# Optimization experiments

Measured on AMD Instinct MI355X. Metric: run time of the kernel, lower is better.

The kernel has to match this reference:

```python
import jax, jax.numpy as jnp
import numpy as np

N = 100000
FEAT = 256
HID = 128
OUT = 64
E = 1600000


def setup_inputs() -> dict:
    key = jax.random.key(0)
    ks = jax.random.split(key, 8)
    x = jax.random.normal(ks[0], (N, FEAT), dtype=jnp.float32)
    edge_index = jax.random.randint(ks[1], (2, E), 0, N, dtype=jnp.int64)
    # Glorot-like weights, zero bias (PyG GCNConv default init style)
    def glorot(k, fin, fout):
        s = (6.0 / (fin + fout)) ** 0.5
        return jax.random.uniform(k, (fin, fout), jnp.float32, -s, s)
    return {
        "x": x,
        "edge_index": edge_index,
        "W1": glorot(ks[2], FEAT, HID), "b1": jnp.zeros((HID,), jnp.float32),
        "W2": glorot(ks[3], HID, HID), "b2": jnp.zeros((HID,), jnp.float32),
        "W3": glorot(ks[4], HID, OUT), "b3": jnp.zeros((OUT,), jnp.float32),
    }


def _gcn_prep(edge_index, n_nodes):
    # Add self-loops and compute symmetric normalization deg^-1/2 (PyG gcn_norm).
    loops = jnp.arange(n_nodes, dtype=edge_index.dtype)
    src = jnp.concatenate([edge_index[0], loops])
    dst = jnp.concatenate([edge_index[1], loops])
    ones = jnp.ones(src.shape[0], dtype=jnp.float32)
    deg = jax.ops.segment_sum(ones, dst, num_segments=n_nodes)
    dinv = jnp.where(deg > 0, jax.lax.rsqrt(jnp.maximum(deg, 1.0)), 0.0)
    norm = dinv[src] * dinv[dst]  # [E+N]
    return src, dst, norm


def _gcn_layer(x, src, dst, norm, W, b, n_nodes):
    h = x @ W                              # [N, F_out]
    msg = h[src] * norm[:, None]           # gather + edge scale
    out = jax.ops.segment_sum(msg, dst, num_segments=n_nodes)  # scatter-add
    return out + b


def reference(x, edge_index, W1, b1, W2, b2, W3, b3):
    n = x.shape[0]
    src, dst, norm = _gcn_prep(edge_index, n)
    h = jax.nn.relu(_gcn_layer(x, src, dst, norm, W1, b1, n))
    h = jax.nn.relu(_gcn_layer(h, src, dst, norm, W2, b2, n))
    return _gcn_layer(h, src, dst, norm, W3, b3, n)
```

## Files before the change

kernel.cpp:

```cpp
#include <hip/hip_runtime.h>
#include <hip/hip_bf16.h>


#define NNODES 100000
#define NB 391
#define PB 2048
#define BCAP 12288

typedef _Float16 half8  __attribute__((ext_vector_type(8)));
typedef _Float16 half4v __attribute__((ext_vector_type(4)));
typedef float    floatx4 __attribute__((ext_vector_type(4)));

static __device__ __forceinline__ floatx4 h2f4(half4v v) {
    return (floatx4){(float)v.x, (float)v.y, (float)v.z, (float)v.w};
}
static __device__ __forceinline__ floatx4 h2f4lo(half8 v) {
    return (floatx4){(float)v[0], (float)v[1], (float)v[2], (float)v[3]};
}
static __device__ __forceinline__ floatx4 h2f4hi(half8 v) {
    return (floatx4){(float)v[4], (float)v[5], (float)v[6], (float)v[7]};
}

__global__ __launch_bounds__(256) void blockhist_k(const int* __restrict__ dst,
                                                   int* __restrict__ H, int e) {
    __shared__ int h[NB];
    for (int q = threadIdx.x; q < NB; q += 256) h[q] = 0;
    __syncthreads();
    int base = blockIdx.x * PB;
    int lim = e - base; if (lim > PB) lim = PB;
    for (int i = threadIdx.x; i < lim; i += 256)
        atomicAdd(&h[dst[base + i] >> 8], 1);
    __syncthreads();
    for (int q = threadIdx.x; q < NB; q += 256)
        H[(size_t)blockIdx.x * NB + q] = h[q];
}

__global__ __launch_bounds__(256) void bucketscan_k(const int* __restrict__ H,
                                                    int* __restrict__ O,
                                                    int* __restrict__ T, int npb) {
    __shared__ int lds[256];
    int b = blockIdx.x, t = threadIdx.x;
    int running = 0;
    for (int c0 = 0; c0 < npb; c0 += 256) {
        int idx = c0 + t;
        int v = (idx < npb) ? H[(size_t)idx * NB + b] : 0;
        lds[t] = v;
        __syncthreads();
        #pragma unroll
        for (int off = 1; off < 256; off <<= 1) {
            int u = (t >= off) ? lds[t - off] : 0;
            __syncthreads();
            lds[t] += u;
            __syncthreads();
        }
        int excl = lds[t] - v + running;
        if (idx < npb) O[(size_t)idx * NB + b] = excl;
        running += lds[255];
        __syncthreads();
    }
    if (t == 0) T[b] = running;
}

__global__ __launch_bounds__(512) void scanT_k(const int* __restrict__ T,
                                               int* __restrict__ bbase, int e) {
    __shared__ int lds[512];
    int t = threadIdx.x;
    int v = (t < NB) ? T[t] : 0;
    lds[t] = v;
    __syncthreads();
    #pragma unroll
    for (int off = 1; off < 512; off <<= 1) {
        int u = (t >= off) ? lds[t - off] : 0;
        __syncthreads();
        lds[t] += u;
        __syncthreads();
    }
    if (t < NB) bbase[t] = lds[t] - v;
    if (t == 0) bbase[NB] = e;
}

__global__ __launch_bounds__(256) void scatter_k(const int* __restrict__ src,
                                                 const int* __restrict__ dst,
                                                 const int* __restrict__ O,
                                                 const int* __restrict__ bbase,
                                                 unsigned* __restrict__ binned, int e) {
    __shared__ int cur[NB];
    for (int q = threadIdx.x; q < NB; q += 256)
        cur[q] = bbase[q] + O[(size_t)blockIdx.x * NB + q];
    __syncthreads();
    int base = blockIdx.x * PB;
    int lim = e - base; if (lim > PB) lim = PB;
    for (int i = threadIdx.x; i < lim; i += 256) {
        int d = dst[base + i];
        int s = src[base + i];
        int p = atomicAdd(&cur[d >> 8], 1);
        binned[p] = ((unsigned)(d & 255) << 17) | (unsigned)s;
    }
}

__global__ __launch_bounds__(256) void bucket_fill_k(
    const unsigned* __restrict__ binned, const int* __restrict__ bbase,
    int* __restrict__ rowptr, int* __restrict__ eidx,
    float* __restrict__ dinv, int n, int e) {
    __shared__ int cnt[256];
    __shared__ int cur[256];
    __shared__ int lds[256];
    __shared__ int sbuf[BCAP];
    int b = blockIdx.x, t = threadIdx.x;
    int beg = bbase[b], end = bbase[b + 1];
    int m = end - beg;
    cnt[t] = 0;
    __syncthreads();
    for (int q = t; q < m; q += 256) {
        unsigned r = binned[beg + q];
        atomicAdd(&cnt[r >> 17], 1);
    }
    __syncthreads();
    int v = cnt[t];
    lds[t] = v;
    __syncthreads();
    #pragma unroll
    for (int off = 1; off < 256; off <<= 1) {
        int u = (t >= off) ? lds[t - off] : 0;
        __syncthreads();
        lds[t] += u;
        __syncthreads();
    }
    int excl = lds[t] - v;
    int node = b * 256 + t;
    if (node < n) {
        rowptr[node] = beg + excl;
        dinv[node] = rsqrtf(1.0f + (float)v);
    }
    if (b == NB - 1 && t == 0) rowptr[n] = e;
    cur[t] = excl;
    __syncthreads();
    for (int q = t; q < m; q += 256) {
        unsigned r = binned[beg + q];
        int p = atomicAdd(&cur[r >> 17], 1);
        if (p < BCAP) sbuf[p] = (int)(r & 0x1FFFFu);
    }
    __syncthreads();
    for (int q = t; q < m; q += 256) eidx[beg + q] = sbuf[q];
}

static __device__ __forceinline__ void cast_frag(
    const float* __restrict__ W, _Float16* __restrict__ Wf,
    int FIN, int FOUT, int i) {
    int k = i / FOUT, n = i % FOUT;
    int ct = n >> 4, mrow = n & 15;
    int kc = k >> 5, hi = (k & 31) >> 3, j = k & 7;
    int NKC = FIN / 32;
    int idx = ((ct * NKC + kc) * 64 + hi * 16 + mrow) * 8 + j;
    Wf[idx] = (_Float16)W[(size_t)k * FOUT + n];
}

__global__ __launch_bounds__(256) void castW_k(
    const float* __restrict__ W1, const float* __restrict__ W2,
    const float* __restrict__ W3, _Float16* __restrict__ Wf1,
    _Float16* __restrict__ Wf2, _Float16* __restrict__ Wf3) {
    int i = blockIdx.x * 256 + threadIdx.x;
    if (i < 256 * 128) cast_frag(W1, Wf1, 256, 128, i);
    if (i < 128 * 128) cast_frag(W2, Wf2, 128, 128, i);
    if (i < 128 * 64)  cast_frag(W3, Wf3, 128, 64, i);
}

template<typename TA, int FIN, int FOUT>
__global__ __launch_bounds__(256, 2) void gemm_ldsB_k(
    const TA* __restrict__ X, const _Float16* __restrict__ Wf,
    const float* __restrict__ dinv, _Float16* __restrict__ G, int n)
{
    constexpr int NKC = FIN / 32;
    constexpr int NCT = FOUT / 16;
    __shared__ _Float16 wS[FOUT * FIN];

    const int tid  = threadIdx.x;
    const int wave = tid >> 6;
    const int lane = tid & 63;
    const int mrow = lane & 15;
    const int kq   = (lane >> 4) * 8;

    {
        const half8* s = (const half8*)Wf;
        half8* d = (half8*)wS;
        constexpr int TOT8 = FOUT * FIN / 8;
        #pragma unroll
        for (int i = tid; i < TOT8; i += 256) d[i] = s[i];
    }

    int r = blockIdx.x * 64 + wave * 16 + mrow;
    if (r > n - 1) r = n - 1;

    half8 af[NKC];
    if constexpr (sizeof(TA) == 4) {
        const float* xp = (const float*)X + (size_t)r * FIN + kq;
        float4 t0[NKC], t1[NKC];
        #pragma unroll
        for (int kc = 0; kc < NKC; ++kc) {
            t0[kc] = *(const float4*)(xp + kc * 32);
            t1[kc] = *(const float4*)(xp + kc * 32 + 4);
        }
        #pragma unroll
        for (int kc = 0; kc < NKC; ++kc) {
            float4 u0 = t0[kc], u1 = t1[kc];
            af[kc] = (half8){(_Float16)u0.x, (_Float16)u0.y, (_Float16)u0.z, (_Float16)u0.w,
                             (_Float16)u1.x, (_Float16)u1.y, (_Float16)u1.z, (_Float16)u1.w};
        }
    } else {
        const _Float16* xp = (const _Float16*)X + (size_t)r * FIN + kq;
        #pragma unroll
        for (int kc = 0; kc < NKC; ++kc)
            af[kc] = *(const half8*)(xp + kc * 32);
    }

    __syncthreads();

    floatx4 acc[NCT];
    #pragma unroll
    for (int ct = 0; ct < NCT; ++ct) acc[ct] = (floatx4){0.f, 0.f, 0.f, 0.f};

    #pragma unroll
    for (int kc = 0; kc < NKC; ++kc) {
        #pragma unroll
        for (int ct = 0; ct < NCT; ++ct) {
            half8 bf = *(const half8*)&wS[(((ct * NKC) + kc) * 64 + lane) * 8];
            acc[ct] = __builtin_amdgcn_mfma_f32_16x16x32_f16(af[kc], bf, acc[ct], 0, 0, 0);
        }
    }

    int rbase = blockIdx.x * 64 + wave * 16 + (lane >> 4) * 4;
    #pragma unroll
    for (int reg = 0; reg < 4; ++reg) {
        int rr = rbase + reg;
        if (rr < n) {
            float s = dinv[rr];
            #pragma unroll
            for (int ct = 0; ct < NCT; ++ct)
                G[(size_t)rr * FOUT + ct * 16 + mrow] = (_Float16)(acc[ct][reg] * s);
        }
    }
}

template<bool RELU>
__global__ __launch_bounds__(256) void gatherq128_k(
    const _Float16* __restrict__ g, const int* __restrict__ rowptr,
    const int* __restrict__ eidx, const float* __restrict__ dinv,
    const float* __restrict__ bias, _Float16* __restrict__ out, int n)
{
    const int wave = threadIdx.x >> 6;
    const int lane = threadIdx.x & 63;
    const int q = lane >> 4;
    const int f = lane & 15;
    const int node = blockIdx.x * 4 + wave;
    if (node >= n) return;

    const int beg = rowptr[node];
    const int end = rowptr[node + 1];

    const half8* g8 = (const half8*)g;
    floatx4 aA0 = {0.f,0.f,0.f,0.f}, aA1 = aA0, aB0 = aA0, aB1 = aA0;
    {
        half8 v = g8[(size_t)node * 16 + f];
        if (q == 0) { aA0 = h2f4lo(v); aA1 = h2f4hi(v); }
    }

    for (int j0 = beg; j0 < end; j0 += 64) {
        int m = end - j0; if (m > 64) m = 64;
        int id = (lane < m) ? __builtin_nontemporal_load(eidx + j0 + lane) : 0;
        int t = 0;
        for (; t + 15 < m; t += 16) {
            int i0 = __shfl(id, t + q);
            int i1 = __shfl(id, t + 4 + q);
            int i2 = __shfl(id, t + 8 + q);
            int i3 = __shfl(id, t + 12 + q);
            half8 v0 = g8[(size_t)i0 * 16 + f];
            half8 v1 = g8[(size_t)i1 * 16 + f];
            half8 v2 = g8[(size_t)i2 * 16 + f];
            half8 v3 = g8[(size_t)i3 * 16 + f];
            aA0 += h2f4lo(v0); aA1 += h2f4hi(v0);
            aB0 += h2f4lo(v1); aB1 += h2f4hi(v1);
            aA0 += h2f4lo(v2); aA1 += h2f4hi(v2);
            aB0 += h2f4lo(v3); aB1 += h2f4hi(v3);
        }
        for (; t < m; t += 4) {
            int e = t + q;
            int i0 = __shfl(id, e & 63);
            half8 v0 = g8[(size_t)i0 * 16 + f];
            if (e < m) { aA0 += h2f4lo(v0); aA1 += h2f4hi(v0); }
        }
    }

    aA0 += aB0; aA1 += aB1;
    #pragma unroll
    for (int off = 16; off <= 32; off <<= 1) {
        aA0.x += __shfl_xor(aA0.x, off);
        aA0.y += __shfl_xor(aA0.y, off);
        aA0.z += __shfl_xor(aA0.z, off);
        aA0.w += __shfl_xor(aA0.w, off);
        aA1.x += __shfl_xor(aA1.x, off);
        aA1.y += __shfl_xor(aA1.y, off);
        aA1.z += __shfl_xor(aA1.z, off);
        aA1.w += __shfl_xor(aA1.w, off);
    }

    if (q == 0) {
        float sc = dinv[node];
        float4 b0 = *(const float4*)(bias + 8 * f);
        float4 b1 = *(const float4*)(bias + 8 * f + 4);
        float o0 = fmaf(aA0.x, sc, b0.x);
        float o1 = fmaf(aA0.y, sc, b0.y);
        float o2 = fmaf(aA0.z, sc, b0.z);
        float o3 = fmaf(aA0.w, sc, b0.w);
        float o4 = fmaf(aA1.x, sc, b1.x);
        float o5 = fmaf(aA1.y, sc, b1.y);
        float o6 = fmaf(aA1.z, sc, b1.z);
        float o7 = fmaf(aA1.w, sc, b1.w);
        if (RELU) {
            o0 = fmaxf(o0, 0.f); o1 = fmaxf(o1, 0.f);
            o2 = fmaxf(o2, 0.f); o3 = fmaxf(o3, 0.f);
            o4 = fmaxf(o4, 0.f); o5 = fmaxf(o5, 0.f);
            o6 = fmaxf(o6, 0.f); o7 = fmaxf(o7, 0.f);
        }
        half8 hv = {(_Float16)o0, (_Float16)o1, (_Float16)o2, (_Float16)o3,
                    (_Float16)o4, (_Float16)o5, (_Float16)o6, (_Float16)o7};
        __builtin_nontemporal_store(hv, (half8*)out + (size_t)node * 16 + f);
    }
}

__global__ __launch_bounds__(256) void gatherq64_k(
    const _Float16* __restrict__ g, const int* __restrict__ rowptr,
    const int* __restrict__ eidx, const float* __restrict__ dinv,
    const float* __restrict__ bias, float* __restrict__ out, int n)
{
    const int wave = threadIdx.x >> 6;
    const int lane = threadIdx.x & 63;
    const int q = lane >> 4;
    const int f = lane & 15;
    const int node = blockIdx.x * 4 + wave;
    if (node >= n) return;

    const int beg = rowptr[node];
    const int end = rowptr[node + 1];

    const half4v* g4 = (const half4v*)g;
    floatx4 aA = {0.f,0.f,0.f,0.f}, aB = aA;
    {
        half4v v = g4[(size_t)node * 16 + f];
        if (q == 0) aA = h2f4(v);
    }

    for (int j0 = beg; j0 < end; j0 += 64) {
        int m = end - j0; if (m > 64) m = 64;
        int id = (lane < m) ? __builtin_nontemporal_load(eidx + j0 + lane) : 0;
        int t = 0;
        for (; t + 15 < m; t += 16) {
            int i0 = __shfl(id, t + q);
            int i1 = __shfl(id, t + 4 + q);
            int i2 = __shfl(id, t + 8 + q);
            int i3 = __shfl(id, t + 12 + q);
            half4v v0 = g4[(size_t)i0 * 16 + f];
            half4v v1 = g4[(size_t)i1 * 16 + f];
            half4v v2 = g4[(size_t)i2 * 16 + f];
            half4v v3 = g4[(size_t)i3 * 16 + f];
            aA += h2f4(v0); aB += h2f4(v1);
            aA += h2f4(v2); aB += h2f4(v3);
        }
        for (; t < m; t += 4) {
            int e = t + q;
            int i0 = __shfl(id, e & 63);
            half4v v0 = g4[(size_t)i0 * 16 + f];
            if (e < m) aA += h2f4(v0);
        }
    }

    aA += aB;
    #pragma unroll
    for (int off = 16; off <= 32; off <<= 1) {
        aA.x += __shfl_xor(aA.x, off);
        aA.y += __shfl_xor(aA.y, off);
        aA.z += __shfl_xor(aA.z, off);
        aA.w += __shfl_xor(aA.w, off);
    }

    if (q == 0) {
        float sc = dinv[node];
        float4 bb = *(const float4*)(bias + 4 * f);
        floatx4 o;
        o.x = fmaf(aA.x, sc, bb.x);
        o.y = fmaf(aA.y, sc, bb.y);
        o.z = fmaf(aA.z, sc, bb.z);
        o.w = fmaf(aA.w, sc, bb.w);
        __builtin_nontemporal_store(o, (floatx4*)(out + (size_t)node * 64 + 4 * f));
    }
}

extern "C" void kernel_launch(void* const* d_in, const int* in_sizes, int n_in,
                              void* d_out, int out_size, void* d_ws, size_t ws_size,
                              hipStream_t stream) {
    const float* x  = (const float*)d_in[0];
    const int*   ei = (const int*)d_in[1];
    const float* W1 = (const float*)d_in[2];
    const float* b1 = (const float*)d_in[3];
    const float* W2 = (const float*)d_in[4];
    const float* b2 = (const float*)d_in[5];
    const float* W3 = (const float*)d_in[6];
    const float* b3 = (const float*)d_in[7];
    float* out = (float*)d_out;

    const int N = NNODES;
    const int E = in_sizes[1] / 2;
    const int* srcI = ei;
    const int* dstI = ei + E;

    const int npb = (E + PB - 1) / PB;

    char* ws = (char*)d_ws;
    size_t p = 0;
    auto alloc = [&](size_t bytes) { void* r = ws + p; p = (p + bytes + 255) & ~(size_t)255; return r; };
    float*     dinv   = (float*)    alloc((size_t)N * 4);
    int*       rowptr = (int*)      alloc((size_t)(N + 1) * 4);
    int*       bbase  = (int*)      alloc((size_t)(NB + 1) * 4);
    int*       T      = (int*)      alloc((size_t)NB * 4);
    int*       H      = (int*)      alloc((size_t)npb * NB * 4);
    int*       O      = (int*)      alloc((size_t)npb * NB * 4);
    unsigned*  binned = (unsigned*) alloc((size_t)E * 4);
    int*       eidx   = (int*)      alloc((size_t)E * 4);
    _Float16*  Wf1    = (_Float16*) alloc((size_t)128 * 256 * 2);
    _Float16*  Wf2    = (_Float16*) alloc((size_t)128 * 128 * 2);
    _Float16*  Wf3    = (_Float16*) alloc((size_t)64 * 128 * 2);
    _Float16*  A      = (_Float16*) alloc((size_t)N * 128 * 2);
    _Float16*  Ch     = (_Float16*) alloc((size_t)N * 128 * 2);

    const int nb_node4 = (N + 3) / 4;
    const int nb_gemm  = (N + 63) / 64;

    blockhist_k<<<npb, 256, 0, stream>>>(dstI, H, E);
    castW_k<<<128, 256, 0, stream>>>(W1, W2, W3, Wf1, Wf2, Wf3);
    bucketscan_k<<<NB, 256, 0, stream>>>(H, O, T, npb);
    scanT_k<<<1, 512, 0, stream>>>(T, bbase, E);
    scatter_k<<<npb, 256, 0, stream>>>(srcI, dstI, O, bbase, binned, E);
    bucket_fill_k<<<NB, 256, 0, stream>>>(binned, bbase, rowptr, eidx, dinv, N, E);

    gemm_ldsB_k<float, 256, 128><<<nb_gemm, 256, 0, stream>>>(x, Wf1, dinv, A, N);
    gatherq128_k<true><<<nb_node4, 256, 0, stream>>>(A, rowptr, eidx, dinv, b1, Ch, N);

    gemm_ldsB_k<_Float16, 128, 128><<<nb_gemm, 256, 0, stream>>>(Ch, Wf2, dinv, A, N);
    gatherq128_k<true><<<nb_node4, 256, 0, stream>>>(A, rowptr, eidx, dinv, b2, Ch, N);

    gemm_ldsB_k<_Float16, 128, 64><<<nb_gemm, 256, 0, stream>>>(Ch, Wf3, dinv, A, N);
    gatherq64_k<<<nb_node4, 256, 0, stream>>>(A, rowptr, eidx, dinv, b3, out, N);
}
```

Measured before the change: 452.3 us.

## Make GEMM kernels persistent with prefetch of next row tile

Turns the three per-layer GEMM kernels into persistent kernels with a fixed grid (512 or 1024 blocks) that loop over 64-row tiles. The W fragment is loaded into LDS once per block instead of once per tile. The next tile's A rows are loaded into registers while the current tile's MFMAs run, hiding global load latency. The cost is higher register pressure from the prefetch buffers, and the launch-bounds occupancy hint now varies per layer.

```diff
diff --git a/kernel.cpp b/kernel.cpp
--- a/kernel.cpp
+++ b/kernel.cpp
@@ -165,8 +165,8 @@
     if (i < 128 * 64)  cast_frag(W3, Wf3, 128, 64, i);
 }
 
-template<typename TA, int FIN, int FOUT>
-__global__ __launch_bounds__(256, 2) void gemm_ldsB_k(
+template<typename TA, int FIN, int FOUT, int WPE>
+__global__ __launch_bounds__(256, WPE) void gemm_persist_k(
     const TA* __restrict__ X, const _Float16* __restrict__ Wf,
     const float* __restrict__ dinv, _Float16* __restrict__ G, int n)
 {
@@ -180,6 +180,27 @@
     const int mrow = lane & 15;
     const int kq   = (lane >> 4) * 8;
 
+    float4 t0[NKC], t1[NKC];
+    half8  araw[NKC];
+
+    auto issueA = [&](int tile) {
+        int r = tile * 64 + wave * 16 + mrow;
+        if (r > n - 1) r = n - 1;
+        if constexpr (sizeof(TA) == 4) {
+            const float* xp = (const float*)X + (size_t)r * FIN + kq;
+            #pragma unroll
+            for (int kc = 0; kc < NKC; ++kc) {
+                t0[kc] = *(const float4*)(xp + kc * 32);
+                t1[kc] = *(const float4*)(xp + kc * 32 + 4);
+            }
+        } else {
+            const _Float16* xp = (const _Float16*)X + (size_t)r * FIN + kq;
+            #pragma unroll
+            for (int kc = 0; kc < NKC; ++kc)
+                araw[kc] = *(const half8*)(xp + kc * 32);
+        }
+    };
+
     {
         const half8* s = (const half8*)Wf;
         half8* d = (half8*)wS;
@@ -187,56 +208,50 @@
         #pragma unroll
         for (int i = tid; i < TOT8; i += 256) d[i] = s[i];
     }
-
-    int r = blockIdx.x * 64 + wave * 16 + mrow;
-    if (r > n - 1) r = n - 1;
-
-    half8 af[NKC];
-    if constexpr (sizeof(TA) == 4) {
-        const float* xp = (const float*)X + (size_t)r * FIN + kq;
-        float4 t0[NKC], t1[NKC];
+    issueA(blockIdx.x);
+    __syncthreads();
+
+    const int ntiles = (n + 63) >> 6;
+    for (int tile = blockIdx.x; tile < ntiles; tile += gridDim.x) {
+        half8 af[NKC];
+        if constexpr (sizeof(TA) == 4) {
+            #pragma unroll
+            for (int kc = 0; kc < NKC; ++kc) {
+                float4 u0 = t0[kc], u1 = t1[kc];
+                af[kc] = (half8){(_Float16)u0.x, (_Float16)u0.y, (_Float16)u0.z, (_Float16)u0.w,
+                                 (_Float16)u1.x, (_Float16)u1.y, (_Float16)u1.z, (_Float16)u1.w};
+            }
+        } else {
+            #pragma unroll
+            for (int kc = 0; kc < NKC; ++kc) af[kc] = araw[kc];
+        }
+
+        int tn = tile + gridDim.x;
+        if (tn < ntiles) issueA(tn);
+
+        floatx4 acc[NCT];
+        #pragma unroll
+        for (int ct = 0; ct < NCT; ++ct) acc[ct] = (floatx4){0.f, 0.f, 0.f, 0.f};
+
         #pragma unroll
         for (int kc = 0; kc < NKC; ++kc) {
-            t0[kc] = *(const float4*)(xp + kc * 32);
-            t1[kc] = *(const float4*)(xp + kc * 32 + 4);
-        }
+            #pragma unroll
+            for (int ct = 0; ct < NCT; ++ct) {
+                half8 bf = *(const half8*)&wS[(((ct * NKC) + kc) * 64 + lane) * 8];
+                acc[ct] = __builtin_amdgcn_mfma_f32_16x16x32_f16(af[kc], bf, acc[ct], 0, 0, 0);
+            }
+        }
+
+        int rbase = tile * 64 + wave * 16 + (lane >> 4) * 4;
         #pragma unroll
-        for (int kc = 0; kc < NKC; ++kc) {
-            float4 u0 = t0[kc], u1 = t1[kc];
-            af[kc] = (half8){(_Float16)u0.x, (_Float16)u0.y, (_Float16)u0.z, (_Float16)u0.w,
-                             (_Float16)u1.x, (_Float16)u1.y, (_Float16)u1.z, (_Float16)u1.w};
-        }
-    } else {
-        const _Float16* xp = (const _Float16*)X + (size_t)r * FIN + kq;
-        #pragma unroll
-        for (int kc = 0; kc < NKC; ++kc)
-            af[kc] = *(const half8*)(xp + kc * 32);
-    }
-
-    __syncthreads();
-
-    floatx4 acc[NCT];
-    #pragma unroll
-    for (int ct = 0; ct < NCT; ++ct) acc[ct] = (floatx4){0.f, 0.f, 0.f, 0.f};
-
-    #pragma unroll
-    for (int kc = 0; kc < NKC; ++kc) {
-        #pragma unroll
-        for (int ct = 0; ct < NCT; ++ct) {
-            half8 bf = *(const half8*)&wS[(((ct * NKC) + kc) * 64 + lane) * 8];
-            acc[ct] = __builtin_amdgcn_mfma_f32_16x16x32_f16(af[kc], bf, acc[ct], 0, 0, 0);
-        }
-    }
-
-    int rbase = blockIdx.x * 64 + wave * 16 + (lane >> 4) * 4;
-    #pragma unroll
-    for (int reg = 0; reg < 4; ++reg) {
-        int rr = rbase + reg;
-        if (rr < n) {
-            float s = dinv[rr];
-            #pragma unroll
-            for (int ct = 0; ct < NCT; ++ct)
-                G[(size_t)rr * FOUT + ct * 16 + mrow] = (_Float16)(acc[ct][reg] * s);
+        for (int reg = 0; reg < 4; ++reg) {
+            int rr = rbase + reg;
+            if (rr < n) {
+                float s = dinv[rr];
+                #pragma unroll
+                for (int ct = 0; ct < NCT; ++ct)
+                    G[(size_t)rr * FOUT + ct * 16 + mrow] = (_Float16)(acc[ct][reg] * s);
+            }
         }
     }
 }
@@ -432,7 +447,8 @@
     _Float16*  Ch     = (_Float16*) alloc((size_t)N * 128 * 2);
 
     const int nb_node4 = (N + 3) / 4;
-    const int nb_gemm  = (N + 63) / 64;
+    const int GP2 = 512;
+    const int GP4 = 1024;
 
     blockhist_k<<<npb, 256, 0, stream>>>(dstI, H, E);
     castW_k<<<128, 256, 0, stream>>>(W1, W2, W3, Wf1, Wf2, Wf3);
@@ -441,12 +457,12 @@
     scatter_k<<<npb, 256, 0, stream>>>(srcI, dstI, O, bbase, binned, E);
     bucket_fill_k<<<NB, 256, 0, stream>>>(binned, bbase, rowptr, eidx, dinv, N, E);
 
-    gemm_ldsB_k<float, 256, 128><<<nb_gemm, 256, 0, stream>>>(x, Wf1, dinv, A, N);
+    gemm_persist_k<float, 256, 128, 2><<<GP2, 256, 0, stream>>>(x, Wf1, dinv, A, N);
     gatherq128_k<true><<<nb_node4, 256, 0, stream>>>(A, rowptr, eidx, dinv, b1, Ch, N);
 
-    gemm_ldsB_k<_Float16, 128, 128><<<nb_gemm, 256, 0, stream>>>(Ch, Wf2, dinv, A, N);
+    gemm_persist_k<_Float16, 128, 128, 4><<<GP4, 256, 0, stream>>>(Ch, Wf2, dinv, A, N);
     gatherq128_k<true><<<nb_node4, 256, 0, stream>>>(A, rowptr, eidx, dinv, b2, Ch, N);
 
-    gemm_ldsB_k<_Float16, 128, 64><<<nb_gemm, 256, 0, stream>>>(Ch, Wf3, dinv, A, N);
+    gemm_persist_k<_Float16, 128, 64, 4><<<GP4, 256, 0, stream>>>(Ch, Wf3, dinv, A, N);
     gatherq64_k<<<nb_node4, 256, 0, stream>>>(A, rowptr, eidx, dinv, b3, out, N);
 }
```

After: 523.4 us. 15.7% more time.

## Replace two-level bucket sort CSR build with global atomic histogram and scatter

Applied to the files above, without the earlier changes.

Replaces the bucketed radix-style CSR construction (per-block histograms, bucket scan, binned scatter, per-bucket LDS fill) with a per-node global atomic degree histogram, a two-level scan, and a direct atomic-cursor scatter of source indices into CSR order. This drops the intermediate binned array and the H/O tables, and zeroes the degree buffer inside the weight-cast kernel. In exchange it uses 1.6M global atomics twice, and edge order within each row becomes nondeterministic, which can cause small floating-point differences in the aggregation and worse locality in the gather.

```diff
diff --git a/kernel.cpp b/kernel.cpp
--- a/kernel.cpp
+++ b/kernel.cpp
@@ -4,8 +4,6 @@
 
 #define NNODES 100000
 #define NB 391
-#define PB 2048
-#define BCAP 12288
 
 typedef _Float16 half8  __attribute__((ext_vector_type(8)));
 typedef _Float16 half4v __attribute__((ext_vector_type(4)));
@@ -19,129 +17,6 @@
 }
 static __device__ __forceinline__ floatx4 h2f4hi(half8 v) {
     return (floatx4){(float)v[4], (float)v[5], (float)v[6], (float)v[7]};
-}
-
-__global__ __launch_bounds__(256) void blockhist_k(const int* __restrict__ dst,
-                                                   int* __restrict__ H, int e) {
-    __shared__ int h[NB];
-    for (int q = threadIdx.x; q < NB; q += 256) h[q] = 0;
-    __syncthreads();
-    int base = blockIdx.x * PB;
-    int lim = e - base; if (lim > PB) lim = PB;
-    for (int i = threadIdx.x; i < lim; i += 256)
-        atomicAdd(&h[dst[base + i] >> 8], 1);
-    __syncthreads();
-    for (int q = threadIdx.x; q < NB; q += 256)
-        H[(size_t)blockIdx.x * NB + q] = h[q];
-}
-
-__global__ __launch_bounds__(256) void bucketscan_k(const int* __restrict__ H,
-                                                    int* __restrict__ O,
-                                                    int* __restrict__ T, int npb) {
-    __shared__ int lds[256];
-    int b = blockIdx.x, t = threadIdx.x;
-    int running = 0;
-    for (int c0 = 0; c0 < npb; c0 += 256) {
-        int idx = c0 + t;
-        int v = (idx < npb) ? H[(size_t)idx * NB + b] : 0;
-        lds[t] = v;
-        __syncthreads();
-        #pragma unroll
-        for (int off = 1; off < 256; off <<= 1) {
-            int u = (t >= off) ? lds[t - off] : 0;
-            __syncthreads();
-            lds[t] += u;
-            __syncthreads();
-        }
-        int excl = lds[t] - v + running;
-        if (idx < npb) O[(size_t)idx * NB + b] = excl;
-        running += lds[255];
-        __syncthreads();
-    }
-    if (t == 0) T[b] = running;
-}
-
-__global__ __launch_bounds__(512) void scanT_k(const int* __restrict__ T,
-                                               int* __restrict__ bbase, int e) {
-    __shared__ int lds[512];
-    int t = threadIdx.x;
-    int v = (t < NB) ? T[t] : 0;
-    lds[t] = v;
-    __syncthreads();
-    #pragma unroll
-    for (int off = 1; off < 512; off <<= 1) {
-        int u = (t >= off) ? lds[t - off] : 0;
-        __syncthreads();
-        lds[t] += u;
-        __syncthreads();
-    }
-    if (t < NB) bbase[t] = lds[t] - v;
-    if (t == 0) bbase[NB] = e;
-}
-
-__global__ __launch_bounds__(256) void scatter_k(const int* __restrict__ src,
-                                                 const int* __restrict__ dst,
-                                                 const int* __restrict__ O,
-                                                 const int* __restrict__ bbase,
-                                                 unsigned* __restrict__ binned, int e) {
-    __shared__ int cur[NB];
-    for (int q = threadIdx.x; q < NB; q += 256)
-        cur[q] = bbase[q] + O[(size_t)blockIdx.x * NB + q];
-    __syncthreads();
-    int base = blockIdx.x * PB;
-    int lim = e - base; if (lim > PB) lim = PB;
-    for (int i = threadIdx.x; i < lim; i += 256) {
-        int d = dst[base + i];
-        int s = src[base + i];
-        int p = atomicAdd(&cur[d >> 8], 1);
-        binned[p] = ((unsigned)(d & 255) << 17) | (unsigned)s;
-    }
-}
-
-__global__ __launch_bounds__(256) void bucket_fill_k(
-    const unsigned* __restrict__ binned, const int* __restrict__ bbase,
-    int* __restrict__ rowptr, int* __restrict__ eidx,
-    float* __restrict__ dinv, int n, int e) {
-    __shared__ int cnt[256];
-    __shared__ int cur[256];
-    __shared__ int lds[256];
-    __shared__ int sbuf[BCAP];
-    int b = blockIdx.x, t = threadIdx.x;
-    int beg = bbase[b], end = bbase[b + 1];
-    int m = end - beg;
-    cnt[t] = 0;
-    __syncthreads();
-    for (int q = t; q < m; q += 256) {
-        unsigned r = binned[beg + q];
-        atomicAdd(&cnt[r >> 17], 1);
-    }
-    __syncthreads();
-    int v = cnt[t];
-    lds[t] = v;
-    __syncthreads();
-    #pragma unroll
-    for (int off = 1; off < 256; off <<= 1) {
-        int u = (t >= off) ? lds[t - off] : 0;
-        __syncthreads();
-        lds[t] += u;
-        __syncthreads();
-    }
-    int excl = lds[t] - v;
-    int node = b * 256 + t;
-    if (node < n) {
-        rowptr[node] = beg + excl;
-        dinv[node] = rsqrtf(1.0f + (float)v);
-    }
-    if (b == NB - 1 && t == 0) rowptr[n] = e;
-    cur[t] = excl;
-    __syncthreads();
-    for (int q = t; q < m; q += 256) {
-        unsigned r = binned[beg + q];
-        int p = atomicAdd(&cur[r >> 17], 1);
-        if (p < BCAP) sbuf[p] = (int)(r & 0x1FFFFu);
-    }
-    __syncthreads();
-    for (int q = t; q < m; q += 256) eidx[beg + q] = sbuf[q];
 }
 
 static __device__ __forceinline__ void cast_frag(
@@ -155,14 +30,91 @@
     Wf[idx] = (_Float16)W[(size_t)k * FOUT + n];
 }
 
-__global__ __launch_bounds__(256) void castW_k(
+__global__ __launch_bounds__(256) void castWz_k(
     const float* __restrict__ W1, const float* __restrict__ W2,
     const float* __restrict__ W3, _Float16* __restrict__ Wf1,
-    _Float16* __restrict__ Wf2, _Float16* __restrict__ Wf3) {
+    _Float16* __restrict__ Wf2, _Float16* __restrict__ Wf3,
+    int* __restrict__ deg) {
     int i = blockIdx.x * 256 + threadIdx.x;
+    for (int q = i; q < NNODES; q += 128 * 256) deg[q] = 0;
     if (i < 256 * 128) cast_frag(W1, Wf1, 256, 128, i);
     if (i < 128 * 128) cast_frag(W2, Wf2, 128, 128, i);
     if (i < 128 * 64)  cast_frag(W3, Wf3, 128, 64, i);
+}
+
+__global__ __launch_bounds__(256) void hist_k(const int* __restrict__ dst,
+                                              int* __restrict__ deg, int e) {
+    int i0 = blockIdx.x * 256 + threadIdx.x;
+    int stride = gridDim.x * 256;
+    for (int i = i0; i < e; i += stride)
+        atomicAdd(&deg[__builtin_nontemporal_load(dst + i)], 1);
+}
+
+__global__ __launch_bounds__(256) void blockscan_k(const int* __restrict__ deg,
+                                                   int* __restrict__ rowloc,
+                                                   int* __restrict__ T, int n) {
+    __shared__ int lds[256];
+    int b = blockIdx.x, t = threadIdx.x;
+    int node = b * 256 + t;
+    int v = (node < n) ? deg[node] : 0;
+    lds[t] = v;
+    __syncthreads();
+    #pragma unroll
+    for (int off = 1; off < 256; off <<= 1) {
+        int u = (t >= off) ? lds[t - off] : 0;
+        __syncthreads();
+        lds[t] += u;
+        __syncthreads();
+    }
+    if (node < n) rowloc[node] = lds[t] - v;
+    if (t == 255) T[b] = lds[255];
+}
+
+__global__ __launch_bounds__(512) void scanT_k(const int* __restrict__ T,
+                                               int* __restrict__ bbase, int e) {
+    __shared__ int lds[512];
+    int t = threadIdx.x;
+    int v = (t < NB) ? T[t] : 0;
+    lds[t] = v;
+    __syncthreads();
+    #pragma unroll
+    for (int off = 1; off < 512; off <<= 1) {
+        int u = (t >= off) ? lds[t - off] : 0;
+        __syncthreads();
+        lds[t] += u;
+        __syncthreads();
+    }
+    if (t < NB) bbase[t] = lds[t] - v;
+    if (t == 0) bbase[NB] = e;
+}
+
+__global__ __launch_bounds__(256) void finalize_k(
+    const int* __restrict__ deg, const int* __restrict__ rowloc,
+    const int* __restrict__ bbase, int* __restrict__ rowptr,
+    int* __restrict__ cursor, float* __restrict__ dinv, int n, int e) {
+    int b = blockIdx.x, t = threadIdx.x;
+    int node = b * 256 + t;
+    if (node < n) {
+        int rp = bbase[b] + rowloc[node];
+        rowptr[node] = rp;
+        cursor[node] = rp;
+        dinv[node] = rsqrtf(1.0f + (float)deg[node]);
+    }
+    if (b == NB - 1 && t == 0) rowptr[n] = e;
+}
+
+__global__ __launch_bounds__(256) void scatterg_k(const int* __restrict__ src,
+                                                  const int* __restrict__ dst,
+                                                  int* __restrict__ cursor,
+                                                  int* __restrict__ eidx, int e) {
+    int i0 = blockIdx.x * 256 + threadIdx.x;
+    int stride = gridDim.x * 256;
+    for (int i = i0; i < e; i += stride) {
+        int d = __builtin_nontemporal_load(dst + i);
+        int s = __builtin_nontemporal_load(src + i);
+        int p = atomicAdd(&cursor[d], 1);
+        eidx[p] = s;
+    }
 }
 
 template<typename TA, int FIN, int FOUT>
@@ -412,8 +364,6 @@
     const int* srcI = ei;
     const int* dstI = ei + E;
 
-    const int npb = (E + PB - 1) / PB;
-
     char* ws = (char*)d_ws;
     size_t p = 0;
     auto alloc = [&](size_t bytes) { void* r = ws + p; p = (p + bytes + 255) & ~(size_t)255; return r; };
@@ -421,9 +371,9 @@
     int*       rowptr = (int*)      alloc((size_t)(N + 1) * 4);
     int*       bbase  = (int*)      alloc((size_t)(NB + 1) * 4);
     int*       T      = (int*)      alloc((size_t)NB * 4);
-    int*       H      = (int*)      alloc((size_t)npb * NB * 4);
-    int*       O      = (int*)      alloc((size_t)npb * NB * 4);
-    unsigned*  binned = (unsigned*) alloc((size_t)E * 4);
+    int*       deg    = (int*)      alloc((size_t)N * 4);
+    int*       rowloc = (int*)      alloc((size_t)N * 4);
+    int*       cursor = (int*)      alloc((size_t)N * 4);
     int*       eidx   = (int*)      alloc((size_t)E * 4);
     _Float16*  Wf1    = (_Float16*) alloc((size_t)128 * 256 * 2);
     _Float16*  Wf2    = (_Float16*) alloc((size_t)128 * 128 * 2);
@@ -434,12 +384,12 @@
     const int nb_node4 = (N + 3) / 4;
     const int nb_gemm  = (N + 63) / 64;
 
-    blockhist_k<<<npb, 256, 0, stream>>>(dstI, H, E);
-    castW_k<<<128, 256, 0, stream>>>(W1, W2, W3, Wf1, Wf2, Wf3);
-    bucketscan_k<<<NB, 256, 0, stream>>>(H, O, T, npb);
+    castWz_k<<<128, 256, 0, stream>>>(W1, W2, W3, Wf1, Wf2, Wf3, deg);
+    hist_k<<<1024, 256, 0, stream>>>(dstI, deg, E);
+    blockscan_k<<<NB, 256, 0, stream>>>(deg, rowloc, T, N);
     scanT_k<<<1, 512, 0, stream>>>(T, bbase, E);
-    scatter_k<<<npb, 256, 0, stream>>>(srcI, dstI, O, bbase, binned, E);
-    bucket_fill_k<<<NB, 256, 0, stream>>>(binned, bbase, rowptr, eidx, dinv, N, E);
+    finalize_k<<<NB, 256, 0, stream>>>(deg, rowloc, bbase, rowptr, cursor, dinv, N, E);
+    scatterg_k<<<1024, 256, 0, stream>>>(srcI, dstI, cursor, eidx, E);
 
     gemm_ldsB_k<float, 256, 128><<<nb_gemm, 256, 0, stream>>>(x, Wf1, dinv, A, N);
     gatherq128_k<true><<<nb_node4, 256, 0, stream>>>(A, rowptr, eidx, dinv, b1, Ch, N);
```

Measured after the change: 585.5 us. 29.4% more time.
